# Kernel optimization log

Measured on AMD Instinct MI355X. Metric: run time of the kernel, lower is better.

Reference implementation:

```python
import jax, jax.numpy as jnp
import numpy as np

B, L, N, DM = 32, 12, 883, 64
DSP, DTP, H, HID, HOR = 128, 128, 4, 64, 12
E_SPA = 14128
ENC_LAYERS = 3
HIDDEN = 5 * HID  # 2*embed + node + tid + diw = 320


def _gat(x, es, et, W, a_s, a_d, bias, edge_att=None):
    # GATConv-style attention with optional per-edge info-bottleneck mask (gat_ib)
    n = x.shape[0]
    h = (x @ W).reshape(n, H, -1)            # [n,H,Dh]
    sc_s = (h * a_s).sum(-1)                 # [n,H]
    sc_d = (h * a_d).sum(-1)
    al = jax.nn.leaky_relu(sc_s[es] + sc_d[et], 0.2)   # [E,H]
    al = al - jax.ops.segment_max(al, et, num_segments=n)[et]
    ex = jnp.exp(al)
    a = ex / jax.ops.segment_sum(ex, et, num_segments=n)[et]
    if edge_att is not None:
        a = a * edge_att[:, None]
    out = jax.ops.segment_sum(a[..., None] * h[es], et, num_segments=n)
    return out.reshape(n, -1) + bias


def _gsat(x, ei, gat_p, ext_p):
    # GSAT: embed -> extractor MLP on edge endpoint pairs -> sigmoid edge att -> masked conv
    es, et = ei[0], ei[1]
    emb = _gat(x, es, et, *gat_p)
    w1, b1, w2, b2, w3, b3 = ext_p
    f = jnp.concatenate([emb[es], emb[et]], axis=-1)
    logit = (jax.nn.relu(jax.nn.relu(f @ w1 + b1) @ w2 + b2) @ w3 + b3)[:, 0]
    att = jax.nn.sigmoid(logit)  # eval-mode (no concrete-relaxation sampling)
    return _gat(x, es, et, *gat_p, edge_att=att)


def setup_inputs():
    key = jax.random.key(0)
    ks = iter(jax.random.split(key, 80))
    def nrm(shape, s=0.02):
        return jax.random.normal(next(ks), shape, jnp.float32) * s
    hist = jax.random.normal(next(ks), (B, L, N, 3), jnp.float32)
    tid = jax.random.randint(next(ks), (B, L, N), 0, 288).astype(jnp.float32)
    diw = jax.random.randint(next(ks), (B, L, N), 0, 7).astype(jnp.float32)
    hist = hist.at[..., 1].set(tid).at[..., 2].set(diw)
    ei_spa = jax.random.randint(next(ks), (2, E_SPA), 0, N).astype(jnp.int32)
    g = jnp.arange(L, dtype=jnp.int32)
    ei_temp = jnp.stack([jnp.repeat(g, L), jnp.tile(g, L)])  # dense lag x lag temporal graph
    inp = dict(history_data=hist, edge_idx_spa=ei_spa, edge_idx_temp=ei_temp)
    inp.update(
        node_emb=nrm((N, HID)), tid_emb=nrm((288, HID)), diw_emb=nrm((7, HID)),
        start_w=nrm((3, DM)), start_b=jnp.zeros((DM,), jnp.float32),
        ts_w=nrm((DM * L, HID)), ts_b=jnp.zeros((HID,), jnp.float32),
        tr_spat_w=nrm((L * DM, DSP)), tr_spat_b=jnp.zeros((DSP,), jnp.float32),
        inv_spat_w=nrm((DSP, L * DM)), inv_spat_b=jnp.zeros((L * DM,), jnp.float32),
        tr_temp_w=nrm((N * DM, DTP)), tr_temp_b=jnp.zeros((DTP,), jnp.float32),
        inv_temp_w=nrm((DTP, N * DM)), inv_temp_b=jnp.zeros((N * DM,), jnp.float32),
        gat_sp_w=nrm((DSP, DSP)), gat_sp_asrc=nrm((H, DSP // H)), gat_sp_adst=nrm((H, DSP // H)), gat_sp_bias=jnp.zeros((DSP,), jnp.float32),
        ext_sp_w1=nrm((2 * DSP, 4 * DSP)), ext_sp_b1=jnp.zeros((4 * DSP,), jnp.float32),
        ext_sp_w2=nrm((4 * DSP, DSP)), ext_sp_b2=jnp.zeros((DSP,), jnp.float32),
        ext_sp_w3=nrm((DSP, 1)), ext_sp_b3=jnp.zeros((1,), jnp.float32),
        gat_tp_w=nrm((DTP, DTP)), gat_tp_asrc=nrm((H, DTP // H)), gat_tp_adst=nrm((H, DTP // H)), gat_tp_bias=jnp.zeros((DTP,), jnp.float32),
        ext_tp_w1=nrm((2 * DTP, 4 * DTP)), ext_tp_b1=jnp.zeros((4 * DTP,), jnp.float32),
        ext_tp_w2=nrm((4 * DTP, DTP)), ext_tp_b2=jnp.zeros((DTP,), jnp.float32),
        ext_tp_w3=nrm((DTP, 1)), ext_tp_b3=jnp.zeros((1,), jnp.float32),
        enc_w1=nrm((ENC_LAYERS, HIDDEN, HIDDEN)), enc_b1=jnp.zeros((ENC_LAYERS, HIDDEN), jnp.float32),
        enc_w2=nrm((ENC_LAYERS, HIDDEN, HIDDEN)), enc_b2=jnp.zeros((ENC_LAYERS, HIDDEN), jnp.float32),
        reg_w=nrm((HIDDEN, HOR)), reg_b=jnp.zeros((HOR,), jnp.float32),
    )
    return inp


def reference(history_data, edge_idx_spa, edge_idx_temp, node_emb, tid_emb, diw_emb,
              start_w, start_b, ts_w, ts_b,
              tr_spat_w, tr_spat_b, inv_spat_w, inv_spat_b,
              tr_temp_w, tr_temp_b, inv_temp_w, inv_temp_b,
              gat_sp_w, gat_sp_asrc, gat_sp_adst, gat_sp_bias,
              ext_sp_w1, ext_sp_b1, ext_sp_w2, ext_sp_b2, ext_sp_w3, ext_sp_b3,
              gat_tp_w, gat_tp_asrc, gat_tp_adst, gat_tp_bias,
              ext_tp_w1, ext_tp_b1, ext_tp_w2, ext_tp_b2, ext_tp_w3, ext_tp_b3,
              enc_w1, enc_b1, enc_w2, enc_b2, reg_w, reg_b):
    b, l, n = history_data.shape[:3]
    tid = jax.lax.stop_gradient(history_data[:, -1, :, 1]).astype(jnp.int32)
    diw = jax.lax.stop_gradient(history_data[:, -1, :, 2]).astype(jnp.int32)
    X = history_data[..., :3] @ start_w + start_b           # [B,L,N,DM]
    res = X.transpose(0, 2, 1, 3).reshape(b, n, l * DM)      # [B,N,L*DM]
    ts_res = res @ ts_w + ts_b                               # conv1x1 over nodes == per-node linear
    gp_sp = (gat_sp_w, gat_sp_asrc, gat_sp_adst, gat_sp_bias)
    ep_sp = (ext_sp_w1, ext_sp_b1, ext_sp_w2, ext_sp_b2, ext_sp_w3, ext_sp_b3)
    gp_tp = (gat_tp_w, gat_tp_asrc, gat_tp_adst, gat_tp_bias)
    ep_tp = (ext_tp_w1, ext_tp_b1, ext_tp_w2, ext_tp_b2, ext_tp_w3, ext_tp_b3)
    # batch_st_gsat: per-sample spatial GSAT then temporal GSAT (vmapped instead of Python loop)
    spa_in = res @ tr_spat_w + tr_spat_b                     # [B,N,DSP]
    spa_out = jax.vmap(lambda xx: _gsat(xx, edge_idx_spa, gp_sp, ep_sp))(spa_in)
    spa_back = (spa_out @ inv_spat_w + inv_spat_b).reshape(b, n, l, DM).transpose(0, 2, 1, 3)
    temp_in = spa_back.reshape(b, l, n * DM) @ tr_temp_w + tr_temp_b   # [B,L,DTP]
    temp_out = jax.vmap(lambda xx: _gsat(xx, edge_idx_temp, gp_tp, ep_tp))(temp_in)
    temp_back = (temp_out @ inv_temp_w + inv_temp_b).reshape(b, l, n, DM)
    ts_temp = temp_back.transpose(0, 2, 1, 3).reshape(b, n, l * DM) @ ts_w + ts_b
    hid = jnp.concatenate([
        ts_res, ts_temp,
        jnp.broadcast_to(node_emb, (b, n, HID)),
        tid_emb[tid], diw_emb[diw],
    ], axis=-1)                                              # [B,N,320]
    for i in range(ENC_LAYERS):  # MLP_res: x + fc2(relu(fc1(x)))
        hid = hid + jax.nn.relu(hid @ enc_w1[i] + enc_b1[i]) @ enc_w2[i] + enc_b2[i]
    pred = hid @ reg_w + reg_b                               # [B,N,HOR]
    return pred.transpose(0, 2, 1)[..., None]                # [B,HOR,N,1]
```

## Files before the change

kernel.cpp:

```cpp
#include <hip/hip_runtime.h>
#include <hip/hip_bf16.h>
#include <cstdint>
#include <cstddef>

#define B_   32
#define L_   12
#define N_   883
#define DM_  64
#define E_SP 14128
#define E_TP 144
#define NT_  12
#define RBN  28256
#define RBL  384
#define LDM  768
#define NDM  56512

static inline int cdiv_h(int a, int b){ return (a+b-1)/b; }

__device__ __forceinline__ ushort f2bf(float f){
    unsigned u = __float_as_uint(f);
    unsigned lsb = (u >> 16) & 1u;
    u += 0x7fffu + lsb;
    return (ushort)(u >> 16);
}
__device__ __forceinline__ float bf2f(ushort h){
    return __uint_as_float(((unsigned)h) << 16);
}
__device__ __forceinline__ ushort f2h(float f){
    _Float16 h = (_Float16)f;
    ushort r; __builtin_memcpy(&r, &h, 2);
    return r;
}

typedef __bf16 bf16x8 __attribute__((ext_vector_type(8)));
typedef _Float16 f16x8 __attribute__((ext_vector_type(8)));
typedef _Float16 f16x2 __attribute__((ext_vector_type(2)));
typedef float  f32x4  __attribute__((ext_vector_type(4)));
typedef short  s16x2  __attribute__((ext_vector_type(2)));
union BF8 { bf16x8 v; ushort u[8]; unsigned w[4]; int4 i; };
union HF8 { f16x8 v; ushort u[8]; unsigned w[4]; int4 i; };

__device__ __forceinline__ unsigned pkrelu(unsigned x){
    s16x2 v;
    __builtin_memcpy(&v, &x, 4);
    s16x2 z = 0;
    v = __builtin_elementwise_max(v, z);
    unsigned r;
    __builtin_memcpy(&r, &v, 4);
    return r;
}
__device__ __forceinline__ unsigned pkaddh(unsigned x, unsigned y){
    f16x2 a, b;
    __builtin_memcpy(&a, &x, 4);
    __builtin_memcpy(&b, &y, 4);
    a = a + b;
    unsigned r;
    __builtin_memcpy(&r, &a, 4);
    return r;
}

__global__ void k_mkA(const float* __restrict__ sw, const float* __restrict__ sb,
                      const float* __restrict__ tsw, const float* __restrict__ tsb,
                      const float* __restrict__ trsp, const float* __restrict__ trspb,
                      float* __restrict__ A1, float* __restrict__ A2,
                      float* __restrict__ cb1, float* __restrict__ cb2)
{
    int idx = blockIdx.x*256 + threadIdx.x;
    if (idx < 36*64) {
        int k = idx >> 6, h = idx & 63;
        int l = k/3, c = k - l*3;
        float s = 0.f;
        #pragma unroll 8
        for (int d = 0; d < 64; ++d) s += sw[c*64+d]*tsw[(size_t)(l*64+d)*64 + h];
        A1[idx] = s;
    } else if (idx < 36*64 + 36*128) {
        int i = idx - 36*64;
        int k = i >> 7, p = i & 127;
        int l = k/3, c = k - l*3;
        float s = 0.f;
        #pragma unroll 8
        for (int d = 0; d < 64; ++d) s += sw[c*64+d]*trsp[(size_t)(l*64+d)*128 + p];
        A2[i] = s;
    } else if (idx < 36*64 + 36*128 + 64) {
        int h = idx - (36*64 + 36*128);
        float s = tsb[h];
        #pragma unroll 8
        for (int k = 0; k < 768; ++k) s += sb[k & 63]*tsw[(size_t)k*64 + h];
        cb1[h] = s;
    } else if (idx < 36*64 + 36*128 + 64 + 128) {
        int p = idx - (36*64 + 36*128 + 64);
        float s = trspb[p];
        #pragma unroll 8
        for (int k = 0; k < 768; ++k) s += sb[k & 63]*trsp[(size_t)k*128 + p];
        cb2[p] = s;
    }
}
__global__ void k_front(const float* __restrict__ hist, const float* __restrict__ A1,
                        const float* __restrict__ A2, const float* __restrict__ cb1,
                        const float* __restrict__ cb2, float* __restrict__ ts_res,
                        ushort* __restrict__ spa_in)
{
    int idx = blockIdx.x*256 + threadIdx.x;
    if (idx >= RBN*192) return;
    int bn = idx / 192, h = idx - bn*192;
    int b = bn / N_, n = bn - b*N_;
    const float* hp = hist + ((size_t)(b*L_)*N_ + n)*3;
    bool isTs = (h < 64);
    int hh = isTs ? h : (h - 64);
    int stride = isTs ? 64 : 128;
    const float* A = isTs ? (A1 + hh) : (A2 + hh);
    float acc = isTs ? cb1[hh] : cb2[hh];
    #pragma unroll
    for (int l = 0; l < 12; ++l) {
        float x0 = hp[l*2649 + 0];
        float x1 = hp[l*2649 + 1];
        float x2 = hp[l*2649 + 2];
        acc += x0*A[(l*3+0)*stride] + x1*A[(l*3+1)*stride] + x2*A[(l*3+2)*stride];
    }
    if (isTs) ts_res[(size_t)bn*64 + hh] = acc;
    else      spa_in[(size_t)bn*128 + hh] = f2bf(acc);
}

template<int CT, int AMODE, int EPI, bool RELU, bool RES>
__launch_bounds__(256)
__global__ void mgemm(const ushort* __restrict__ A, const ushort* __restrict__ WT,
                      const float* __restrict__ bias, float* __restrict__ resF,
                      void* __restrict__ outP, int M, int N, int K)
{
    const int t = threadIdx.x, wv = t >> 6, l = t & 63;
    const int lr = l & 15, lk = l >> 4;
    const int row0 = blockIdx.y*64 + wv*16;
    const int col0 = blockIdx.x * (CT*16);
    int arr = row0 + lr; if (arr >= M) arr = M-1;
    int ab = 0, an = 0;
    if (AMODE == 1) { ab = arr / N_; an = arr - ab*N_; }
    const ushort* ap = A + (size_t)arr*K + lk*8;
    f32x4 acc[CT] = {};
    for (int k0 = 0; k0 < K; k0 += 32) {
        BF8 af;
        if (AMODE == 0) af.i = *(const int4*)(ap + k0);
        else {
            int k = k0 + lk*8; int ll = k >> 6, d = k & 63;
            af.i = *(const int4*)(A + ((size_t)(ab*L_ + ll))*NDM + (size_t)an*64 + d);
        }
        #pragma unroll
        for (int ct = 0; ct < CT; ++ct) {
            BF8 bf; bf.i = *(const int4*)&WT[(size_t)(col0 + ct*16 + lr)*K + k0 + lk*8];
            acc[ct] = __builtin_amdgcn_mfma_f32_16x16x32_bf16(af.v, bf.v, acc[ct], 0, 0, 0);
        }
    }
    #pragma unroll
    for (int ct = 0; ct < CT; ++ct) {
        int c = col0 + ct*16 + lr;
        float bv = 0.f;
        if (EPI == 2) { if (bias && c < 12) bv = bias[c]; }
        else if (bias) bv = bias[c];
        #pragma unroll
        for (int g = 0; g < 4; ++g) {
            int r = row0 + lk*4 + g;
            if (r >= M) continue;
            float v = acc[ct][g] + bv;
            if (RELU) v = fmaxf(v, 0.f);
            if (RES) {
                v += resF[(size_t)r*N + c];
                resF[(size_t)r*N + c] = v;
            }
            if (EPI == 0) {
                ((ushort*)outP)[(size_t)r*N + c] = f2bf(v);
            } else if (EPI == 1) {
                ((float*)outP)[(size_t)r*N + c] = v;
            } else if (EPI == 2) {
                if (c < 12) {
                    int b = r / N_, n = r - (r/N_)*N_;
                    ((float*)outP)[((size_t)(b*L_ + c))*N_ + n] = v;
                }
            } else {
                int b = r / N_, n = r - (r/N_)*N_;
                ((ushort*)outP)[((size_t)(b*L_ + (c>>6)))*NDM + (size_t)n*64 + (c&63)] = f2bf(v);
            }
        }
    }
}

template<int RT, int CT, int EPI, bool RELU, bool RES>
__launch_bounds__(256)
__global__ void mgemm_rt(const ushort* __restrict__ A, const ushort* __restrict__ WT,
                         const float* __restrict__ bias, float* __restrict__ resF,
                         void* __restrict__ outP, int M, int N, int K)
{
    const int t = threadIdx.x, wv = t >> 6, l = t & 63;
    const int lr = l & 15, lk = l >> 4;
    const int rowbase = blockIdx.y*(4*RT*16) + wv*(RT*16);
    const int col0 = blockIdx.x * (CT*16);
    const ushort* ap[RT];
    #pragma unroll
    for (int rt = 0; rt < RT; ++rt) {
        int arr = rowbase + rt*16 + lr; if (arr >= M) arr = M-1;
        ap[rt] = A + (size_t)arr*K + lk*8;
    }
    f32x4 acc[RT][CT] = {};
    for (int k0 = 0; k0 < K; k0 += 32) {
        BF8 af[RT];
        #pragma unroll
        for (int rt = 0; rt < RT; ++rt) af[rt].i = *(const int4*)(ap[rt] + k0);
        #pragma unroll
        for (int ct = 0; ct < CT; ++ct) {
            BF8 bf; bf.i = *(const int4*)&WT[(size_t)(col0 + ct*16 + lr)*K + k0 + lk*8];
            #pragma unroll
            for (int rt = 0; rt < RT; ++rt)
                acc[rt][ct] = __builtin_amdgcn_mfma_f32_16x16x32_bf16(af[rt].v, bf.v,
                                                                     acc[rt][ct], 0, 0, 0);
        }
    }
    #pragma unroll
    for (int rt = 0; rt < RT; ++rt)
        #pragma unroll
        for (int ct = 0; ct < CT; ++ct) {
            int c = col0 + ct*16 + lr;
            float bv = bias ? bias[c] : 0.f;
            #pragma unroll
            for (int g = 0; g < 4; ++g) {
                int r = rowbase + rt*16 + lk*4 + g;
                if (r >= M) continue;
                float v = acc[rt][ct][g] + bv;
                if (RELU) v = fmaxf(v, 0.f);
                if (RES) {
                    v += resF[(size_t)r*N + c];
                    resF[(size_t)r*N + c] = v;
                }
                if (EPI == 0) {
                    ((ushort*)outP)[(size_t)r*N + c] = f2bf(v);
                } else if (EPI == 1) {
                    ((float*)outP)[(size_t)r*N + c] = v;
                } else if (EPI == 4) {
                    ((ushort*)outP)[(size_t)r*N + c] = f2h(v);
                } else {
                    int b = r / N_, n = r - (r/N_)*N_;
                    ((ushort*)outP)[((size_t)(b*L_ + (c>>6)))*NDM + (size_t)n*64 + (c&63)] = f2bf(v);
                }
            }
        }
}

#define TNC 8
__launch_bounds__(256)
__global__ void k_tempIn(const ushort* __restrict__ spaB, const ushort* __restrict__ ispWT,
                         const float* __restrict__ isb, const ushort* __restrict__ WtT,
                         float* __restrict__ out)
{
    __shared__ ushort T1[16*768];
    const int t = threadIdx.x, wv = t >> 6, l = t & 63;
    const int lr = l & 15, lk = l >> 4;
    const int bh = blockIdx.y;
    const int n0 = blockIdx.x * TNC;
    const int nEnd = (n0 + TNC < N_) ? n0 + TNC : N_;

    f32x4 acc2[3][8] = {};
    for (int n = n0; n < nEnd; ++n) {
        f32x4 acc1[12] = {};
        for (int k0 = 0; k0 < 128; k0 += 32) {
            BF8 af; af.i = *(const int4*)&spaB[((size_t)(bh*16 + lr)*N_ + n)*128 + k0 + lk*8];
            #pragma unroll
            for (int ct = 0; ct < 12; ++ct) {
                BF8 bf; bf.i = *(const int4*)&ispWT[(size_t)(wv*192 + ct*16 + lr)*128 + k0 + lk*8];
                acc1[ct] = __builtin_amdgcn_mfma_f32_16x16x32_bf16(af.v, bf.v, acc1[ct], 0, 0, 0);
            }
        }
        __syncthreads();
        #pragma unroll
        for (int ct = 0; ct < 12; ++ct) {
            int c = wv*192 + ct*16 + lr;
            float bv = isb[c];
            int ll = c >> 6, d = c & 63;
            #pragma unroll
            for (int g = 0; g < 4; ++g) {
                int b = lk*4 + g;
                int r = b*12 + ll;
                T1[b*768 + ll*64 + (d ^ ((r & 7) << 3))] = f2bf(acc1[ct][g] + bv);
            }
        }
        __syncthreads();
        #pragma unroll
        for (int kc = 0; kc < 2; ++kc) {
            BF8 bfr[8];
            #pragma unroll
            for (int ct = 0; ct < 8; ++ct)
                bfr[ct].i = *(const int4*)&WtT[(size_t)(ct*16 + lr)*NDM + (size_t)n*64 + kc*32 + lk*8];
            #pragma unroll
            for (int rt = 0; rt < 3; ++rt) {
                int r = wv*48 + rt*16 + lr;
                int b = r / 12, ll = r - b*12;
                int k = kc*32 + lk*8;
                BF8 af;
                af.v = *(const bf16x8*)&T1[b*768 + ll*64 + (k ^ ((r & 7) << 3))];
                #pragma unroll
                for (int ct = 0; ct < 8; ++ct)
                    acc2[rt][ct] = __builtin_amdgcn_mfma_f32_16x16x32_bf16(af.v, bfr[ct].v,
                                                                          acc2[rt][ct], 0, 0, 0);
            }
        }
    }
    #pragma unroll
    for (int rt = 0; rt < 3; ++rt)
        #pragma unroll
        for (int ct = 0; ct < 8; ++ct) {
            int p = ct*16 + lr;
            #pragma unroll
            for (int g = 0; g < 4; ++g) {
                int r = bh*192 + wv*48 + rt*16 + lk*4 + g;
                atomicAdd(&out[(size_t)r*128 + p], acc2[rt][ct][g]);
            }
        }
}

__launch_bounds__(256)
__global__ void k_tsTemp(const ushort* __restrict__ toutB, const ushort* __restrict__ itWT,
                         const float* __restrict__ itb, const ushort* __restrict__ tswT,
                         const float* __restrict__ tsb, float* __restrict__ ts_temp)
{
    __shared__ ushort sb[384*72];
    const int n = blockIdx.x;
    const int t = threadIdx.x, wv = t >> 6, l = t & 63;
    const int lr = l & 15, lk = l >> 4;
    {
        f32x4 acc1[6][4] = {};
        for (int k0 = 0; k0 < 128; k0 += 32) {
            BF8 bfr[4];
            #pragma unroll
            for (int ct = 0; ct < 4; ++ct)
                bfr[ct].i = *(const int4*)&itWT[(size_t)(n*64 + ct*16 + lr)*128 + k0 + lk*8];
            #pragma unroll
            for (int rt = 0; rt < 6; ++rt) {
                BF8 af; af.i = *(const int4*)&toutB[(size_t)(wv*96 + rt*16 + lr)*128 + k0 + lk*8];
                #pragma unroll
                for (int ct = 0; ct < 4; ++ct)
                    acc1[rt][ct] = __builtin_amdgcn_mfma_f32_16x16x32_bf16(af.v, bfr[ct].v,
                                                                          acc1[rt][ct], 0, 0, 0);
            }
        }
        #pragma unroll
        for (int rt = 0; rt < 6; ++rt)
            #pragma unroll
            for (int ct = 0; ct < 4; ++ct) {
                int d = ct*16 + lr;
                float bv = itb[n*64 + d];
                #pragma unroll
                for (int g = 0; g < 4; ++g) {
                    int r = wv*96 + rt*16 + lk*4 + g;
                    int bb = r / 12;
                    sb[r*72 + (d ^ ((bb & 7) << 3))] = f2bf(acc1[rt][ct][g] + bv);
                }
            }
    }
    __syncthreads();
    f32x4 acc2[2] = {};
    #pragma unroll 2
    for (int j = 0; j < 24; ++j) {
        BF8 bfm; bfm.i = *(const int4*)&tswT[(size_t)(wv*16 + lr)*768 + j*32 + lk*8];
        int lidx = j >> 1;
        int koff = (j & 1)*32 + lk*8;
        #pragma unroll
        for (int rt = 0; rt < 2; ++rt) {
            int bb = rt*16 + lr;
            BF8 af;
            af.v = *(const bf16x8*)&sb[(bb*12 + lidx)*72 + (koff ^ ((bb & 7) << 3))];
            acc2[rt] = __builtin_amdgcn_mfma_f32_16x16x32_bf16(af.v, bfm.v, acc2[rt], 0, 0, 0);
        }
    }
    {
        int h = wv*16 + lr;
        float bv = tsb[h];
        #pragma unroll
        for (int rt = 0; rt < 2; ++rt)
            #pragma unroll
            for (int g = 0; g < 4; ++g) {
                int bb = rt*16 + lk*4 + g;
                ts_temp[((size_t)bb*N_ + n)*64 + h] = acc2[rt][g] + bv;
            }
    }
}

__global__ void k_sc(const ushort* __restrict__ h, const float* __restrict__ as_,
                     const float* __restrict__ ad_, float* __restrict__ scs,
                     float* __restrict__ scd, int R)
{
    int r = blockIdx.x*256 + threadIdx.x;
    if (r >= R) return;
    const ushort* hr = h + (size_t)r*128;
    #pragma unroll
    for (int hh = 0; hh < 4; ++hh) {
        float ss = 0.f, sd = 0.f;
        #pragma unroll
        for (int k = 0; k < 32; ++k) {
            float hv = bf2f(hr[hh*32 + k]);
            ss += hv*as_[hh*32+k];
            sd += hv*ad_[hh*32+k];
        }
        scs[(size_t)r*4+hh] = ss;
        scd[(size_t)r*4+hh] = sd;
    }
}

__global__ void k_count(const int* __restrict__ ei, int E, int* __restrict__ counts){
    int e = blockIdx.x*256 + threadIdx.x;
    if (e < E) atomicAdd(&counts[ei[E + e]], 1);
}
__global__ void k_scan(const int* __restrict__ counts, int* __restrict__ off,
                       int* __restrict__ cur, int n)
{
    __shared__ int s[1024];
    int t = threadIdx.x;
    int v0 = (t < n) ? counts[t] : 0;
    s[t] = v0;
    __syncthreads();
    for (int o = 1; o < 1024; o <<= 1) {
        int v = (t >= o) ? s[t-o] : 0;
        __syncthreads();
        s[t] += v;
        __syncthreads();
    }
    if (t < n) {
        off[t+1] = s[t];
        cur[t] = s[t] - v0;
        if (t == 0) off[0] = 0;
    }
}
__global__ void k_fill(const int* __restrict__ ei, int E, int* __restrict__ cur,
                       int* __restrict__ lst){
    int e = blockIdx.x*256 + threadIdx.x;
    if (e < E) {
        int pos = atomicAdd(&cur[ei[E+e]], 1);
        lst[pos] = e;
    }
}

template<bool USE_ATT>
__global__ void k_gather(const ushort* __restrict__ h, const float* __restrict__ scs,
                         const float* __restrict__ scd, const float* __restrict__ att,
                         const int* __restrict__ ei, const int* __restrict__ off,
                         const int* __restrict__ lst, const float* __restrict__ bias,
                         ushort* __restrict__ out, int E, int NN)
{
    int bn = blockIdx.x*4 + (threadIdx.x >> 6);
    int b = bn / NN, n = bn - b*NN;
    int lane = threadIdx.x & 63;
    int c0 = lane*2;
    int hh = lane >> 4;
    float sd = scd[(size_t)bn*4 + hh];
    int o0 = off[n], o1 = off[n+1];
    float ax = 0.f, ay = 0.f, sa = 0.f;
    for (int i = o0; i < o1; ++i) {
        int e = lst[i];
        int s = ei[e];
        float al = scs[(size_t)(b*NN + s)*4 + hh] + sd;
        al = al > 0.f ? al : 0.2f*al;
        float ex = expf(al);
        sa += ex;
        float a = USE_ATT ? ex * att[(size_t)b*E + e] : ex;
        unsigned hv = *(const unsigned*)&h[((size_t)b*NN + s)*128 + c0];
        ax += a * __uint_as_float(hv << 16);
        ay += a * __uint_as_float(hv & 0xffff0000u);
    }
    float rn = (sa > 0.f) ? 1.f/sa : 0.f;
    ushort2 o2;
    o2.x = f2bf(ax*rn + bias[c0]);
    o2.y = f2bf(ay*rn + bias[c0+1]);
    *(ushort2*)&out[(size_t)bn*128 + c0] = o2;
}

__global__ void k_prepW2(const float* __restrict__ W2, ushort* __restrict__ W2T)
{
    int idx = blockIdx.x*256 + threadIdx.x;
    if (idx >= 512*128) return;
    int k = idx >> 7, c = idx & 127;
    W2T[(size_t)c*512 + k] = f2h(W2[idx]);
}
__global__ void k_prepT(const float* __restrict__ W, ushort* __restrict__ WT, int K, int N)
{
    int idx = blockIdx.x*256 + threadIdx.x;
    if (idx >= K*N) return;
    int k = idx / N, c = idx - k*N;
    WT[(size_t)c*K + k] = f2bf(W[idx]);
}
__global__ void k_prepWtT(const float* __restrict__ W, ushort* __restrict__ WT)
{
    __shared__ ushort tile[128][129];
    int k0 = blockIdx.x * 128;
    int t = threadIdx.x;
    for (int i = t; i < 128*128; i += 256) {
        int k = i >> 7, c = i & 127;
        int kk = k0 + k;
        tile[c][k] = (kk < NDM) ? f2bf(W[(size_t)kk*128 + c]) : (ushort)0;
    }
    __syncthreads();
    for (int i = t; i < 128*128; i += 256) {
        int c = i >> 7, k = i & 127;
        int kk = k0 + k;
        if (kk < NDM) WT[(size_t)c*NDM + kk] = tile[c][k];
    }
}
__global__ void k_prepT_big(const float* __restrict__ W, ushort* __restrict__ WT)
{
    __shared__ float tile[128][65];
    int c0 = blockIdx.x * 64;
    int t = threadIdx.x;
    for (int i = t; i < 128*64; i += 256) {
        int k = i >> 6, ci = i & 63;
        tile[k][ci] = W[(size_t)k*NDM + c0 + ci];
    }
    __syncthreads();
    for (int i = t; i < 64*128; i += 256) {
        int ci = i >> 7, k = i & 127;
        WT[(size_t)(c0 + ci)*128 + k] = f2bf(tile[k][ci]);
    }
}
__global__ void k_bcat(const float* __restrict__ b1, float* __restrict__ dst){
    int i = blockIdx.x*256 + threadIdx.x;
    if (i < 1024) dst[i] = (i < 512) ? b1[i] : 0.f;
}

template<bool SWZ>
__launch_bounds__(256, 3)
__global__ void ext2_mfma(const ushort* __restrict__ PQ, const ushort* __restrict__ W2T,
                          const float* __restrict__ b2, const float* __restrict__ w3,
                          const float* __restrict__ b3p, const int* __restrict__ ei,
                          const int* __restrict__ lst,
                          float* __restrict__ att, int E, int NN, int nblk)
{
    __shared__ ushort Bs[2][128*40];
    int bid = blockIdx.x;
    if (SWZ) {
        bid = (blockIdx.x & 7) * (gridDim.x >> 3) + (blockIdx.x >> 3);
        if (bid >= nblk) bid = nblk - 1;
    }
    const int t = threadIdx.x;
    const int wv = t >> 6, l = t & 63;
    const int lr = l & 15, lk = l >> 4;

    const ushort* pr[2]; const ushort* qr[2];
    int row0[2];
    #pragma unroll
    for (int rt = 0; rt < 2; ++rt) {
        row0[rt] = bid*128 + wv*32 + rt*16;
        int r = row0[rt] + lr;
        int b = (int)((unsigned)r / (unsigned)E), i = r - b*E;
        int e = lst[i];
        pr[rt] = PQ + ((size_t)b*NN + ei[e])*1024 + lk*8;
        qr[rt] = PQ + ((size_t)b*NN + ei[E+e])*1024 + 512 + lk*8;
    }
    const int sc = t >> 1, sh = (t & 1) * 16;
    const ushort* wsrc = W2T + (size_t)sc*512 + sh;
    ushort* wd0 = &Bs[0][sc*40 + sh];
    ushort* wd1 = &Bs[1][sc*40 + sh];

    {
        int4 a0 = *(const int4*)(wsrc);
        int4 a1 = *(const int4*)(wsrc + 8);
        *(int4*)wd0 = a0;
        *(int4*)(wd0 + 8) = a1;
    }
    HF8 pu[2], qu[2];
    #pragma unroll
    for (int rt = 0; rt < 2; ++rt) {
        pu[rt].i = *(const int4*)(pr[rt]);
        qu[rt].i = *(const int4*)(qr[rt]);
    }
    int4 bnA = *(const int4*)(wsrc + 32);
    int4 bnB = *(const int4*)(wsrc + 40);
    __syncthreads();

    f32x4 acc[2][8] = {};
    for (int kc = 0; kc < 16; ++kc) {
        const int cb = kc & 1;
        HF8 af[2];
        #pragma unroll
        for (int rt = 0; rt < 2; ++rt)
            #pragma unroll
            for (int j = 0; j < 4; ++j)
                af[rt].w[j] = pkrelu(pkaddh(pu[rt].w[j], qu[rt].w[j]));
        {
            int ka = (kc+1 < 15) ? kc+1 : 15;
            #pragma unroll
            for (int rt = 0; rt < 2; ++rt) {
                pu[rt].i = *(const int4*)(pr[rt] + ka*32);
                qu[rt].i = *(const int4*)(qr[rt] + ka*32);
            }
        }
        __builtin_amdgcn_s_setprio(1);
        #pragma unroll
        for (int ct = 0; ct < 8; ++ct) {
            HF8 bfm;
            bfm.v = *(const f16x8*)&Bs[cb][(ct*16 + lr)*40 + lk*8];
            #pragma unroll
            for (int rt = 0; rt < 2; ++rt)
                acc[rt][ct] = __builtin_amdgcn_mfma_f32_16x16x32_f16(af[rt].v, bfm.v,
                                                                    acc[rt][ct], 0, 0, 0);
        }
        __builtin_amdgcn_s_setprio(0);
        if (kc < 15) {
            ushort* wd = cb ? wd0 : wd1;
            *(int4*)wd = bnA;
            *(int4*)(wd + 8) = bnB;
        }
        {
            int kb = (kc+2 < 15) ? kc+2 : 15;
            bnA = *(const int4*)(wsrc + kb*32);
            bnB = *(const int4*)(wsrc + kb*32 + 8);
        }
        __syncthreads();
    }
    float b3 = b3p[0];
    #pragma unroll
    for (int rt = 0; rt < 2; ++rt) {
        float part[4] = {0.f,0.f,0.f,0.f};
        #pragma unroll
        for (int ct = 0; ct < 8; ++ct) {
            int c = ct*16 + lr;
            float b2v = b2[c], w3v = w3[c];
            #pragma unroll
            for (int g = 0; g < 4; ++g)
                part[g] += fmaxf(acc[rt][ct][g] + b2v, 0.f) * w3v;
        }
        #pragma unroll
        for (int m = 1; m < 16; m <<= 1)
            #pragma unroll
            for (int g = 0; g < 4; ++g)
                part[g] += __shfl_xor(part[g], m, 64);
        if (lr == 0) {
            #pragma unroll
            for (int g = 0; g < 4; ++g) {
                int rr = row0[rt] + lk*4 + g;
                int b = (int)((unsigned)rr / (unsigned)E), i = rr - b*E;
                int e = lst[i];
                att[(size_t)b*E + e] = 1.f/(1.f + expf(-(part[g] + b3)));
            }
        }
    }
}

__global__ void k_bias_fill(float* __restrict__ dst, const float* __restrict__ bias, int n){
    int i = blockIdx.x*256 + threadIdx.x;
    if (i < n) dst[i] = bias[i & 127];
}
__global__ void k_f2b(const float* __restrict__ src, ushort* __restrict__ dst, int n){
    int i = blockIdx.x*256 + threadIdx.x;
    if (i < n) dst[i] = f2bf(src[i]);
}

__global__ void k_hid(const float* __restrict__ ts_res, const float* __restrict__ ts_temp,
                      const float* __restrict__ node_emb, const float* __restrict__ tid_emb,
                      const float* __restrict__ diw_emb, const float* __restrict__ hist,
                      float* __restrict__ hid, ushort* __restrict__ hidB)
{
    int idx = blockIdx.x*256 + threadIdx.x;
    if (idx >= RBN*320) return;
    int r = idx / 320, c = idx - r*320;
    int b = r / N_, n = r - b*N_;
    float v;
    if (c < 64)        v = ts_res[(size_t)r*64 + c];
    else if (c < 128)  v = ts_temp[(size_t)r*64 + (c-64)];
    else if (c < 192)  v = node_emb[(size_t)n*64 + (c-128)];
    else if (c < 256) {
        int tid = (int)hist[((size_t)(b*L_ + (L_-1))*N_ + n)*3 + 1];
        v = tid_emb[(size_t)tid*64 + (c-192)];
    } else {
        int diw = (int)hist[((size_t)(b*L_ + (L_-1))*N_ + n)*3 + 2];
        v = diw_emb[(size_t)diw*64 + (c-256)];
    }
    hid[idx] = v;
    hidB[idx] = f2bf(v);
}

extern "C" void kernel_launch(void* const* d_in, const int* in_sizes, int n_in,
                              void* d_out, int out_size, void* d_ws, size_t ws_size,
                              hipStream_t stream)
{
    (void)in_sizes; (void)n_in; (void)out_size; (void)ws_size;
    const float* hist      = (const float*)d_in[0];
    const int*   ei_sp     = (const int*)  d_in[1];
    const int*   ei_tp     = (const int*)  d_in[2];
    const float* node_emb  = (const float*)d_in[3];
    const float* tid_emb   = (const float*)d_in[4];
    const float* diw_emb   = (const float*)d_in[5];
    const float* start_w   = (const float*)d_in[6];
    const float* start_b   = (const float*)d_in[7];
    const float* ts_w      = (const float*)d_in[8];
    const float* ts_b      = (const float*)d_in[9];
    const float* tr_spat_w = (const float*)d_in[10];
    const float* tr_spat_b = (const float*)d_in[11];
    const float* inv_spat_w= (const float*)d_in[12];
    const float* inv_spat_b= (const float*)d_in[13];
    const float* tr_temp_w = (const float*)d_in[14];
    const float* tr_temp_b = (const float*)d_in[15];
    const float* inv_temp_w= (const float*)d_in[16];
    const float* inv_temp_b= (const float*)d_in[17];
    const float* gat_sp_w  = (const float*)d_in[18];
    const float* gat_sp_as = (const float*)d_in[19];
    const float* gat_sp_ad = (const float*)d_in[20];
    const float* gat_sp_b  = (const float*)d_in[21];
    const float* ext_sp_w1 = (const float*)d_in[22];
    const float* ext_sp_b1 = (const float*)d_in[23];
    const float* ext_sp_w2 = (const float*)d_in[24];
    const float* ext_sp_b2 = (const float*)d_in[25];
    const float* ext_sp_w3 = (const float*)d_in[26];
    const float* ext_sp_b3 = (const float*)d_in[27];
    const float* gat_tp_w  = (const float*)d_in[28];
    const float* gat_tp_as = (const float*)d_in[29];
    const float* gat_tp_ad = (const float*)d_in[30];
    const float* gat_tp_b  = (const float*)d_in[31];
    const float* ext_tp_w1 = (const float*)d_in[32];
    const float* ext_tp_b1 = (const float*)d_in[33];
    const float* ext_tp_w2 = (const float*)d_in[34];
    const float* ext_tp_b2 = (const float*)d_in[35];
    const float* ext_tp_w3 = (const float*)d_in[36];
    const float* ext_tp_b3 = (const float*)d_in[37];
    const float* enc_w1    = (const float*)d_in[38];
    const float* enc_b1    = (const float*)d_in[39];
    const float* enc_w2    = (const float*)d_in[40];
    const float* enc_b2    = (const float*)d_in[41];
    const float* reg_w     = (const float*)d_in[42];
    const float* reg_b     = (const float*)d_in[43];
    float* out = (float*)d_out;

    size_t o = 0;
    char* wsb = (char*)d_ws;
    auto allocB = [&](size_t bytes) -> void* {
        void* p = wsb + o;
        o += (bytes + 255) & ~(size_t)255;
        return p;
    };
    void* bufA = allocB((size_t)RBN*768*2);
    void* bufB = allocB((size_t)RBN*768*2);
    void* bufC = allocB((size_t)RBN*512*2);
    void* bufD = allocB((size_t)RBN*320*2);
    float*  ts_res  = (float*)allocB((size_t)RBN*64*4);
    ushort* spaB    = (ushort*)allocB((size_t)RBN*128*2);
    ushort* hB      = (ushort*)allocB((size_t)RBN*128*2);
    float*  sc_s    = (float*)allocB((size_t)RBN*4*4);
    float*  sc_d    = (float*)allocB((size_t)RBN*4*4);
    float*  att     = (float*)allocB((size_t)B_*E_SP*4);
    ushort* embB    = (ushort*)allocB((size_t)RBN*128*2);
    int*    csr     = (int*)allocB(17024*4);
    float*  temp_in = (float*)allocB((size_t)RBL*128*4);
    ushort* tempB   = (ushort*)allocB((size_t)RBL*128*2);
    ushort* toutB   = (ushort*)allocB((size_t)RBL*128*2);
    ushort* PQ_t    = (ushort*)allocB((size_t)RBL*1024*2);
    float*  ts_temp = (float*)allocB((size_t)RBN*64*4);
    ushort* W2T_sp  = (ushort*)allocB(512*128*2);
    ushort* W2T_tp  = (ushort*)allocB(512*128*2);
    ushort* WtT     = (ushort*)allocB((size_t)128*NDM*2);
    ushort* itWT    = (ushort*)allocB((size_t)NDM*128*2);
    ushort* ispWT   = (ushort*)allocB(768*128*2);
    ushort* gspWT   = (ushort*)allocB(128*128*2);
    ushort* gtpWT   = (ushort*)allocB(128*128*2);
    ushort* w1catT_sp = (ushort*)allocB((size_t)1024*128*2);
    ushort* w1catT_tp = (ushort*)allocB((size_t)1024*128*2);
    float*  b1cat_sp  = (float*)allocB(1024*4);
    float*  b1cat_tp  = (float*)allocB(1024*4);
    ushort* w1T_enc = (ushort*)allocB((size_t)3*320*320*2);
    ushort* w2T_enc = (ushort*)allocB((size_t)3*320*320*2);
    ushort* tswT_hi = (ushort*)allocB(64*768*2);
    ushort* reg_wT  = (ushort*)allocB(16*320*2);
    float*  A1      = (float*)allocB(36*64*4);
    float*  A2      = (float*)allocB(36*128*4);
    float*  cb1     = (float*)allocB(64*4);
    float*  cb2     = (float*)allocB(128*4);

    float*  hid   = (float*)bufA;
    ushort* PQ_sp = (ushort*)bufB;
    ushort* hidB  = (ushort*)bufC;
    ushort* R1b   = (ushort*)bufD;

    int* counts_sp = csr;
    int* off_sp    = csr + 883;
    int* cur_sp    = csr + 1767;
    int* list_sp   = csr + 2650;
    int* counts_tp = csr + 16778;
    int* off_tp    = csr + 16790;
    int* cur_tp    = csr + 16803;
    int* list_tp   = csr + 16815;

    hipMemsetAsync(counts_sp, 0, 883*4, stream);
    k_count<<<cdiv_h(E_SP,256),256,0,stream>>>(ei_sp, E_SP, counts_sp);
    k_scan<<<1,1024,0,stream>>>(counts_sp, off_sp, cur_sp, 883);
    k_fill<<<cdiv_h(E_SP,256),256,0,stream>>>(ei_sp, E_SP, cur_sp, list_sp);
    hipMemsetAsync(counts_tp, 0, 12*4, stream);
    k_count<<<1,256,0,stream>>>(ei_tp, E_TP, counts_tp);
    k_scan<<<1,1024,0,stream>>>(counts_tp, off_tp, cur_tp, 12);
    k_fill<<<1,256,0,stream>>>(ei_tp, E_TP, cur_tp, list_tp);
    k_mkA<<<cdiv_h(36*64+36*128+192,256),256,0,stream>>>(start_w, start_b, ts_w, ts_b,
                                                         tr_spat_w, tr_spat_b,
                                                         A1, A2, cb1, cb2);
    k_prepW2<<<cdiv_h(512*128,256),256,0,stream>>>(ext_sp_w2, W2T_sp);
    k_prepW2<<<cdiv_h(512*128,256),256,0,stream>>>(ext_tp_w2, W2T_tp);
    k_prepWtT<<<cdiv_h(NDM,128),256,0,stream>>>(tr_temp_w, WtT);
    k_prepT_big<<<NDM/64,256,0,stream>>>(inv_temp_w, itWT);
    k_prepT<<<cdiv_h(128*768,256),256,0,stream>>>(inv_spat_w, ispWT, 128, 768);
    k_prepT<<<cdiv_h(128*128,256),256,0,stream>>>(gat_sp_w, gspWT, 128, 128);
    k_prepT<<<cdiv_h(128*128,256),256,0,stream>>>(gat_tp_w, gtpWT, 128, 128);
    k_prepT<<<cdiv_h(128*512,256),256,0,stream>>>(ext_sp_w1,           w1catT_sp,           128, 512);
    k_prepT<<<cdiv_h(128*512,256),256,0,stream>>>(ext_sp_w1 + 128*512, w1catT_sp + 512*128, 128, 512);
    k_prepT<<<cdiv_h(128*512,256),256,0,stream>>>(ext_tp_w1,           w1catT_tp,           128, 512);
    k_prepT<<<cdiv_h(128*512,256),256,0,stream>>>(ext_tp_w1 + 128*512, w1catT_tp + 512*128, 128, 512);
    k_bcat<<<4,256,0,stream>>>(ext_sp_b1, b1cat_sp);
    k_bcat<<<4,256,0,stream>>>(ext_tp_b1, b1cat_tp);
    for (int i = 0; i < 3; ++i) {
        k_prepT<<<cdiv_h(320*320,256),256,0,stream>>>(enc_w1 + (size_t)i*320*320, w1T_enc + (size_t)i*320*320, 320, 320);
        k_prepT<<<cdiv_h(320*320,256),256,0,stream>>>(enc_w2 + (size_t)i*320*320, w2T_enc + (size_t)i*320*320, 320, 320);
    }
    k_prepT<<<cdiv_h(768*64,256),256,0,stream>>>(ts_w, tswT_hi, 768, 64);
    hipMemsetAsync(reg_wT, 0, 16*320*2, stream);
    k_prepT<<<cdiv_h(320*12,256),256,0,stream>>>(reg_w, reg_wT, 320, 12);

    k_front<<<cdiv_h(RBN*192,256),256,0,stream>>>(hist, A1, A2, cb1, cb2, ts_res, spaB);

    mgemm_rt<2,4,0,false,false><<<dim3(2,221),256,0,stream>>>(spaB, gspWT, nullptr, nullptr,
                                                              hB, RBN, 128, 128);
    k_sc<<<cdiv_h(RBN,256),256,0,stream>>>(hB, gat_sp_as, gat_sp_ad, sc_s, sc_d, RBN);
    k_gather<false><<<RBN/4,256,0,stream>>>(hB, sc_s, sc_d, nullptr, ei_sp, off_sp, list_sp,
                                            gat_sp_b, embB, E_SP, N_);
    mgemm_rt<2,8,4,false,false><<<dim3(8,221),256,0,stream>>>(embB, w1catT_sp, b1cat_sp, nullptr,
                                                              PQ_sp, RBN, 1024, 128);
    ext2_mfma<true><<<3536,256,0,stream>>>(PQ_sp, W2T_sp, ext_sp_b2, ext_sp_w3, ext_sp_b3,
                                           ei_sp, list_sp, att, E_SP, N_, (B_*E_SP)/128);
    k_gather<true><<<RBN/4,256,0,stream>>>(hB, sc_s, sc_d, att, ei_sp, off_sp, list_sp,
                                           gat_sp_b, spaB, E_SP, N_);

    k_bias_fill<<<cdiv_h(RBL*128,256),256,0,stream>>>(temp_in, tr_temp_b, RBL*128);
    k_tempIn<<<dim3(cdiv_h(N_,TNC),2),256,0,stream>>>(spaB, ispWT, inv_spat_b, WtT, temp_in);
    k_f2b<<<cdiv_h(RBL*128,256),256,0,stream>>>(temp_in, tempB, RBL*128);

    mgemm_rt<2,4,0,false,false><<<dim3(2,3),256,0,stream>>>(tempB, gtpWT, nullptr, nullptr,
                                                            hB, RBL, 128, 128);
    k_sc<<<cdiv_h(RBL,256),256,0,stream>>>(hB, gat_tp_as, gat_tp_ad, sc_s, sc_d, RBL);
    k_gather<false><<<RBL/4,256,0,stream>>>(hB, sc_s, sc_d, nullptr, ei_tp, off_tp, list_tp,
                                            gat_tp_b, embB, E_TP, NT_);
    mgemm_rt<2,8,4,false,false><<<dim3(8,3),256,0,stream>>>(embB, w1catT_tp, b1cat_tp, nullptr,
                                                            PQ_t, RBL, 1024, 128);
    ext2_mfma<false><<<(B_*E_TP)/128,256,0,stream>>>(PQ_t, W2T_tp, ext_tp_b2, ext_tp_w3,
                                                     ext_tp_b3, ei_tp, list_tp, att, E_TP, NT_,
                                                     (B_*E_TP)/128);
    k_gather<true><<<RBL/4,256,0,stream>>>(hB, sc_s, sc_d, att, ei_tp, off_tp, list_tp,
                                           gat_tp_b, toutB, E_TP, NT_);

    k_tsTemp<<<N_,256,0,stream>>>(toutB, itWT, inv_temp_b, tswT_hi, ts_b, ts_temp);

    k_hid<<<cdiv_h(RBN*320,256),256,0,stream>>>(ts_res, ts_temp, node_emb, tid_emb, diw_emb, hist,
                                                hid, hidB);
    for (int i = 0; i < 3; ++i) {
        mgemm_rt<2,5,0,true,false><<<dim3(4,221),256,0,stream>>>(hidB, w1T_enc + (size_t)i*320*320,
                                                                 enc_b1 + i*320, nullptr, R1b, RBN, 320, 320);
        mgemm_rt<2,5,0,false,true><<<dim3(4,221),256,0,stream>>>(R1b, w2T_enc + (size_t)i*320*320,
                                                                 enc_b2 + i*320, hid, hidB, RBN, 320, 320);
    }
    mgemm<1,0,2,false,false><<<dim3(1,442),256,0,stream>>>(hidB, reg_wT, reg_b, nullptr,
                                                           out, RBN, 16, 320);
}
```

Measured before the change: 1.218 ms.

## Fuse encoder MLP layers into one kernel and parallelize attention score dot products

```diff
diff --git a/kernel.cpp b/kernel.cpp
--- a/kernel.cpp
+++ b/kernel.cpp
@@ -242,6 +242,63 @@
         }
 }
 
+__launch_bounds__(256)
+__global__ void k_encLayer(const ushort* __restrict__ W1T, const float* __restrict__ b1,
+                           const ushort* __restrict__ W2T, const float* __restrict__ b2,
+                           float* __restrict__ hid, ushort* __restrict__ hidB, int M)
+{
+    __shared__ ushort T[64*328];
+    const int t = threadIdx.x, wv = t >> 6, l = t & 63;
+    const int lr = l & 15, lk = l >> 4;
+    const int row0 = blockIdx.x*64 + wv*16;
+    int arr = row0 + lr; if (arr >= M) arr = M-1;
+    const ushort* ap = hidB + (size_t)arr*320 + lk*8;
+    {
+        f32x4 acc[20] = {};
+        for (int k0 = 0; k0 < 320; k0 += 32) {
+            BF8 af; af.i = *(const int4*)(ap + k0);
+            #pragma unroll
+            for (int ct = 0; ct < 20; ++ct) {
+                BF8 bf; bf.i = *(const int4*)&W1T[(size_t)(ct*16 + lr)*320 + k0 + lk*8];
+                acc[ct] = __builtin_amdgcn_mfma_f32_16x16x32_bf16(af.v, bf.v, acc[ct], 0, 0, 0);
+            }
+        }
+        #pragma unroll
+        for (int ct = 0; ct < 20; ++ct) {
+            int c = ct*16 + lr;
+            float bv = b1[c];
+            #pragma unroll
+            for (int g = 0; g < 4; ++g) {
+                int rl = wv*16 + lk*4 + g;
+                T[rl*328 + c] = f2bf(fmaxf(acc[ct][g] + bv, 0.f));
+            }
+        }
+    }
+    __syncthreads();
+    f32x4 acc2[20] = {};
+    for (int k0 = 0; k0 < 320; k0 += 32) {
+        BF8 af; af.v = *(const bf16x8*)&T[(wv*16 + lr)*328 + k0 + lk*8];
+        #pragma unroll
+        for (int ct = 0; ct < 20; ++ct) {
+            BF8 bf; bf.i = *(const int4*)&W2T[(size_t)(ct*16 + lr)*320 + k0 + lk*8];
+            acc2[ct] = __builtin_amdgcn_mfma_f32_16x16x32_bf16(af.v, bf.v, acc2[ct], 0, 0, 0);
+        }
+    }
+    #pragma unroll
+    for (int ct = 0; ct < 20; ++ct) {
+        int c = ct*16 + lr;
+        float bv = b2[c];
+        #pragma unroll
+        for (int g = 0; g < 4; ++g) {
+            int r = row0 + lk*4 + g;
+            if (r >= M) continue;
+            float v = hid[(size_t)r*320 + c] + acc2[ct][g] + bv;
+            hid[(size_t)r*320 + c] = v;
+            hidB[(size_t)r*320 + c] = f2bf(v);
+        }
+    }
+}
+
 #define TNC 8
 __launch_bounds__(256)
 __global__ void k_tempIn(const ushort* __restrict__ spaB, const ushort* __restrict__ ispWT,
@@ -384,20 +441,28 @@
                      const float* __restrict__ ad_, float* __restrict__ scs,
                      float* __restrict__ scd, int R)
 {
-    int r = blockIdx.x*256 + threadIdx.x;
-    if (r >= R) return;
-    const ushort* hr = h + (size_t)r*128;
+    int wid = blockIdx.x*4 + (threadIdx.x >> 6);
+    int l = threadIdx.x & 63;
+    int sub = l >> 4;
+    int j = l & 15;
+    int r = wid*4 + sub;
+    if (r >= R) r = R - 1;
+    BF8 hv; hv.i = *(const int4*)&h[(size_t)r*128 + j*8];
+    int hh = j >> 2;
+    const float* pa = as_ + hh*32 + (j & 3)*8;
+    const float* pd = ad_ + hh*32 + (j & 3)*8;
+    float ss = 0.f, sd = 0.f;
     #pragma unroll
-    for (int hh = 0; hh < 4; ++hh) {
-        float ss = 0.f, sd = 0.f;
-        #pragma unroll
-        for (int k = 0; k < 32; ++k) {
-            float hv = bf2f(hr[hh*32 + k]);
-            ss += hv*as_[hh*32+k];
-            sd += hv*ad_[hh*32+k];
-        }
-        scs[(size_t)r*4+hh] = ss;
-        scd[(size_t)r*4+hh] = sd;
+    for (int k = 0; k < 8; ++k) {
+        float x = bf2f(hv.u[k]);
+        ss += x*pa[k];
+        sd += x*pd[k];
+    }
+    ss += __shfl_xor(ss, 1, 64); ss += __shfl_xor(ss, 2, 64);
+    sd += __shfl_xor(sd, 1, 64); sd += __shfl_xor(sd, 2, 64);
+    if ((j & 3) == 0) {
+        scs[(size_t)r*4 + hh] = ss;
+        scd[(size_t)r*4 + hh] = sd;
     }
 }
 
@@ -769,7 +834,7 @@
     float*  hid   = (float*)bufA;
     ushort* PQ_sp = (ushort*)bufB;
     ushort* hidB  = (ushort*)bufC;
-    ushort* R1b   = (ushort*)bufD;
+    (void)bufD;
 
     int* counts_sp = csr;
     int* off_sp    = csr + 883;
@@ -816,7 +881,7 @@
 
     mgemm_rt<2,4,0,false,false><<<dim3(2,221),256,0,stream>>>(spaB, gspWT, nullptr, nullptr,
                                                               hB, RBN, 128, 128);
-    k_sc<<<cdiv_h(RBN,256),256,0,stream>>>(hB, gat_sp_as, gat_sp_ad, sc_s, sc_d, RBN);
+    k_sc<<<cdiv_h(RBN,16),256,0,stream>>>(hB, gat_sp_as, gat_sp_ad, sc_s, sc_d, RBN);
     k_gather<false><<<RBN/4,256,0,stream>>>(hB, sc_s, sc_d, nullptr, ei_sp, off_sp, list_sp,
                                             gat_sp_b, embB, E_SP, N_);
     mgemm_rt<2,8,4,false,false><<<dim3(8,221),256,0,stream>>>(embB, w1catT_sp, b1cat_sp, nullptr,
@@ -832,7 +897,7 @@
 
     mgemm_rt<2,4,0,false,false><<<dim3(2,3),256,0,stream>>>(tempB, gtpWT, nullptr, nullptr,
                                                             hB, RBL, 128, 128);
-    k_sc<<<cdiv_h(RBL,256),256,0,stream>>>(hB, gat_tp_as, gat_tp_ad, sc_s, sc_d, RBL);
+    k_sc<<<cdiv_h(RBL,16),256,0,stream>>>(hB, gat_tp_as, gat_tp_ad, sc_s, sc_d, RBL);
     k_gather<false><<<RBL/4,256,0,stream>>>(hB, sc_s, sc_d, nullptr, ei_tp, off_tp, list_tp,
                                             gat_tp_b, embB, E_TP, NT_);
     mgemm_rt<2,8,4,false,false><<<dim3(8,3),256,0,stream>>>(embB, w1catT_tp, b1cat_tp, nullptr,
@@ -848,10 +913,9 @@
     k_hid<<<cdiv_h(RBN*320,256),256,0,stream>>>(ts_res, ts_temp, node_emb, tid_emb, diw_emb, hist,
                                                 hid, hidB);
     for (int i = 0; i < 3; ++i) {
-        mgemm_rt<2,5,0,true,false><<<dim3(4,221),256,0,stream>>>(hidB, w1T_enc + (size_t)i*320*320,
-                                                                 enc_b1 + i*320, nullptr, R1b, RBN, 320, 320);
-        mgemm_rt<2,5,0,false,true><<<dim3(4,221),256,0,stream>>>(R1b, w2T_enc + (size_t)i*320*320,
-                                                                 enc_b2 + i*320, hid, hidB, RBN, 320, 320);
+        k_encLayer<<<cdiv_h(RBN,64),256,0,stream>>>(w1T_enc + (size_t)i*320*320, enc_b1 + i*320,
+                                                    w2T_enc + (size_t)i*320*320, enc_b2 + i*320,
+                                                    hid, hidB, RBN);
     }
     mgemm<1,0,2,false,false><<<dim3(1,442),256,0,stream>>>(hidB, reg_wT, reg_b, nullptr,
                                                            out, RBN, 16, 320);
```

Measured after the change: 1.283 ms. +5.3%, slower.
